# Kernel tuning notes

Hardware: AMD Instinct MI355X
Metric: run time of the kernel (lower is better)

Reference implementation:

```python
import jax, jax.numpy as jnp
import numpy as np

NN_SIZE = 10          # k for kNN (includes the point itself as its own nearest neighbor)
COS_EPS = 1e-8        # torch.nn.CosineSimilarity eps


def _pairwise_sqdist(p):
    # p: (B,N,3) -> (B,N,N) squared euclidean distances without (B,N,N,3) intermediate
    x2 = jnp.sum(p * p, axis=-1)                      # (B,N)
    inner = jnp.einsum('bnd,bmd->bnm', p, p)          # (B,N,N)
    return x2[:, :, None] + x2[:, None, :] - 2.0 * inner


def _batch_normals(points):
    # points: (B,N,3) -> PCA normals (B,N,3)
    d = _pairwise_sqdist(points)                      # (B,N,N)
    _, idx = jax.lax.top_k(-d, NN_SIZE)               # (B,N,K) indices of k nearest
    nbrs = jax.vmap(lambda p, i: p[i])(points, idx)   # (B,N,K,3) gathered neighborhoods
    centered = nbrs - jnp.mean(nbrs, axis=2, keepdims=True)
    cov = jnp.einsum('bnki,bnkj->bnij', centered, centered) / NN_SIZE  # (B,N,3,3)
    _, vecs = jnp.linalg.eigh(cov)                    # eigenvalues ascending
    return vecs[..., :, 0]                            # eigvec of smallest eigval = normal


def setup_inputs() -> dict:
    key = jax.random.key(0)
    k1, k2 = jax.random.split(key)
    pred = jax.random.normal(k1, (8, 4096, 3), dtype=jnp.float32)
    gt_normals = jax.random.normal(k2, (8, 4096, 3), dtype=jnp.float32)
    return {"pred": pred, "gt_normals": gt_normals}


def reference(pred, gt_normals):
    pred_normals = _batch_normals(pred)                         # (B,N,3)
    dot = jnp.sum(pred_normals * gt_normals, axis=-1)           # (B,N)
    na = jnp.linalg.norm(pred_normals, axis=-1)
    nb = jnp.linalg.norm(gt_normals, axis=-1)
    cos = dot / (jnp.maximum(na, COS_EPS) * jnp.maximum(nb, COS_EPS))
    return jnp.mean(1.0 - cos)
```

## Files before the change

kernel.cpp:

```cpp
#include <hip/hip_runtime.h>
#include <math.h>


#define NPTS   4096
#define KNN    10
#define NBINS  256
#define XLO    (-5.5f)
#define INVBW  (256.0f / 11.0f)
#define W      1536
#define QPB    16
#define NB     2048
#define LISTCAP 32768

__device__ __forceinline__ unsigned int umed3(unsigned int a, unsigned int b, unsigned int c) {
    unsigned int r;
    asm("v_med3_u32 %0, %1, %2, %3" : "=v"(r) : "v"(a), "v"(b), "v"(c));
    return r;
}

__device__ __forceinline__ void sift(unsigned int nd[KNN], unsigned int key) {
#pragma unroll
    for (int t = KNN - 1; t >= 1; --t)
        nd[t] = umed3(key, nd[t - 1], nd[t]);
    nd[0] = nd[0] < key ? nd[0] : key;
}

__device__ __forceinline__ int xbin(float x) {
    int bin = (int)floorf((x - XLO) * INVBW);
    return bin < 0 ? 0 : (bin > NBINS - 1 ? NBINS - 1 : bin);
}

#define MAKE_KEY(q, c, J)                                                     \
    ({                                                                        \
        float sw_ = (q).w + (c).w;                                            \
        float dp_ = fmaf((q).x, (c).x, fmaf((q).y, (c).y, (q).z * (c).z));    \
        float d_  = fmaf(-2.0f, dp_, sw_);                                    \
        d_ = fmaxf(d_, 0.0f);                                                 \
        (__float_as_uint(d_) & 0xFFFFF000u) | (unsigned)(J);                  \
    })

__device__ float normal_loss3f(const float nbx[KNN], const float nby[KNN],
                               const float nbz[KNN], const float* g3)
{
    float sx = 0.f, sy = 0.f, sz = 0.f;
#pragma unroll
    for (int t = 0; t < KNN; ++t) { sx += nbx[t]; sy += nby[t]; sz += nbz[t]; }
    float mx = sx * 0.1f, my = sy * 0.1f, mz = sz * 0.1f;
    float c00 = 0.f, c01 = 0.f, c02 = 0.f, c11 = 0.f, c12 = 0.f, c22 = 0.f;
#pragma unroll
    for (int t = 0; t < KNN; ++t) {
        float ux = nbx[t] - mx, uy = nby[t] - my, uz = nbz[t] - mz;
        c00 = fmaf(ux, ux, c00);
        c01 = fmaf(ux, uy, c01);
        c02 = fmaf(ux, uz, c02);
        c11 = fmaf(uy, uy, c11);
        c12 = fmaf(uy, uz, c12);
        c22 = fmaf(uz, uz, c22);
    }
    float a00 = c00 * 0.1f, a01 = c01 * 0.1f, a02 = c02 * 0.1f;
    float a11 = c11 * 0.1f, a12 = c12 * 0.1f, a22 = c22 * 0.1f;

    float vx = 1.0f, vy = 0.0f, vz = 0.0f;
    float qd = (a00 + a11 + a22) * (1.0f / 3.0f);
    float p1 = a01 * a01 + a02 * a02 + a12 * a12;
    float b00 = a00 - qd, b11 = a11 - qd, b22 = a22 - qd;
    float p2 = b00 * b00 + b11 * b11 + b22 * b22 + 2.0f * p1;
    if (p2 > 1e-30f) {
        float p   = sqrtf(p2 * (1.0f / 6.0f));
        float inv = 1.0f / p;
        float m00 = b00 * inv, m01 = a01 * inv, m02 = a02 * inv;
        float m11 = b11 * inv, m12 = a12 * inv, m22 = b22 * inv;
        float detB = m00 * (m11 * m22 - m12 * m12)
                   - m01 * (m01 * m22 - m12 * m02)
                   + m02 * (m01 * m12 - m11 * m02);
        float r = 0.5f * detB;
        r = r < -1.0f ? -1.0f : (r > 1.0f ? 1.0f : r);
        float phi  = acosf(r) * (1.0f / 3.0f);
        float eig0 = qd + 2.0f * p * cosf(phi + 2.0943951023931953f);
        float r0x = a00 - eig0, r0y = a01, r0z = a02;
        float r1y = a11 - eig0, r1z = a12;
        float r2z = a22 - eig0;
        float c0x = r0y * r1z - r0z * r1y;
        float c0y = r0z * r0y - r0x * r1z;
        float c0z = r0x * r1y - r0y * r0y;
        float c1x = r0y * r2z - r0z * r1z;
        float c1y = r0z * r0z - r0x * r2z;
        float c1z = r0x * r1z - r0y * r0z;
        float c2x = r1y * r2z - r1z * r1z;
        float c2y = r1z * r0z - r0y * r2z;
        float c2z = r0y * r1z - r1y * r0z;
        float n0 = c0x * c0x + c0y * c0y + c0z * c0z;
        float n1 = c1x * c1x + c1y * c1y + c1z * c1z;
        float n2 = c2x * c2x + c2y * c2y + c2z * c2z;
        float bx, by, bz, bn;
        if (n0 >= n1 && n0 >= n2) { bx = c0x; by = c0y; bz = c0z; bn = n0; }
        else if (n1 >= n2)        { bx = c1x; by = c1y; bz = c1z; bn = n1; }
        else                      { bx = c2x; by = c2y; bz = c2z; bn = n2; }
        if (bn > 1e-30f) {
            float s = rsqrtf(bn);
            vx = bx * s; vy = by * s; vz = bz * s;
        }
    }
    float gx = g3[0], gy = g3[1], gz = g3[2];
    float dotg = vx * gx + vy * gy + vz * gz;
    float na = sqrtf(vx * vx + vy * vy + vz * vz);
    float gn = sqrtf(gx * gx + gy * gy + gz * gz);
    float cs = dotg / (fmaxf(na, 1e-8f) * fmaxf(gn, 1e-8f));
    return 1.0f - cs;
}

__global__ __launch_bounds__(1024) void gtnl_bin(
    const float* __restrict__ pred, float4* __restrict__ wsPts,
    unsigned int* __restrict__ wsBins, unsigned int* __restrict__ wsCnt)
{
    __shared__ unsigned int hist[NBINS];
    __shared__ unsigned int bst[NBINS + 1];

    const int tid = threadIdx.x;
    const int b   = blockIdx.x;
    if (b == 0 && tid == 0) wsCnt[0] = 0;
    const float* src = pred + (size_t)b * NPTS * 3;

    if (tid < NBINS) hist[tid] = 0;
    __syncthreads();

    float px[4], py[4], pz[4];
    int   pb[4], pidx[4];
#pragma unroll
    for (int k = 0; k < 4; ++k) {
        int p = tid + 1024 * k;
        float x = src[3 * p + 0];
        float y = src[3 * p + 1];
        float z = src[3 * p + 2];
        int bin = xbin(x);
        px[k] = x; py[k] = y; pz[k] = z; pb[k] = bin; pidx[k] = p;
        atomicAdd(&hist[bin], 1u);
    }
    __syncthreads();

    if (tid < 64) {
        unsigned s0 = hist[4 * tid + 0], s1 = hist[4 * tid + 1];
        unsigned s2 = hist[4 * tid + 2], s3 = hist[4 * tid + 3];
        unsigned tot = s0 + s1 + s2 + s3;
        unsigned pre = tot;
#pragma unroll
        for (int d = 1; d < 64; d <<= 1) {
            unsigned t = __shfl_up(pre, d, 64);
            if (tid >= d) pre += t;
        }
        unsigned ex = pre - tot;
        bst[4 * tid + 0] = ex;
        bst[4 * tid + 1] = ex + s0;
        bst[4 * tid + 2] = ex + s0 + s1;
        bst[4 * tid + 3] = ex + s0 + s1 + s2;
        if (tid == 63) bst[NBINS] = ex + tot;
    }
    __syncthreads();

    if (tid < NBINS) hist[tid] = bst[tid];
    __syncthreads();

#pragma unroll
    for (int k = 0; k < 4; ++k) {
        unsigned pos = atomicAdd(&hist[pb[k]], 1u);
        wsPts[(size_t)b * NPTS + pos] =
            make_float4(px[k], py[k], pz[k], __uint_as_float((unsigned)pidx[k]));
    }
    if (tid < NBINS) wsBins[b * (NBINS + 1) + tid] = bst[tid];
    if (tid == 0)    wsBins[b * (NBINS + 1) + NBINS] = bst[NBINS];
}

__global__ __launch_bounds__(256, 6) void gtnl_scan(
    const float4* __restrict__ wsPts, const float* __restrict__ gt,
    float* __restrict__ qloss, unsigned int* __restrict__ wsCnt,
    unsigned int* __restrict__ wsList, float* __restrict__ wsThr)
{
    __shared__ float4 pts[W];

    const int tid   = threadIdx.x;
    const int bid   = blockIdx.x;
    const int b     = bid >> 8;
    const int chunk = bid & 255;
    const int qbase = chunk * QPB;
    const int s     = tid & 15;
    const int ql    = tid >> 4;

    int W0 = qbase + QPB / 2 - W / 2;
    W0 = W0 < 0 ? 0 : (W0 > NPTS - W ? NPTS - W : W0);

    const float4* wp = wsPts + (size_t)b * NPTS;
    for (int i = tid; i < W; i += 256) {
        float4 v = wp[W0 + i];
        pts[i] = make_float4(v.x, v.y, v.z, fmaf(v.x, v.x, fmaf(v.y, v.y, v.z * v.z)));
    }
    __syncthreads();

    const int qpos = qbase + ql;
    const float4 q = pts[qpos - W0];

    unsigned int nd[KNN];
#pragma unroll
    for (int t = 0; t < KNN; ++t) nd[t] = 0x7F000000u;

#pragma unroll 8
    for (int t = 0; t < W / 16; ++t) {
        int j = 16 * t + s;
        float4 c = pts[j];
        sift(nd, MAKE_KEY(q, c, j));
    }

#pragma unroll
    for (int r = 1; r <= 8; r <<= 1) {
        unsigned int tmp[KNN];
#pragma unroll
        for (int t = 0; t < KNN; ++t) tmp[t] = nd[t];
#pragma unroll
        for (int t = 0; t < KNN; ++t) {
            unsigned int pk = (unsigned int)__shfl_xor((int)tmp[t], r, 64);
            sift(nd, pk);
        }
    }

    unsigned int thr_bits = (nd[KNN - 1] & 0xFFFFF000u) + 0x1000u;
    float thr = __uint_as_float(thr_bits);
    float hw  = __uint_as_float(__float_as_uint(sqrtf(thr)) + 4) + 1e-3f;
    bool okL = (W0 == 0)        || (q.x - hw > pts[0].x);
    bool okR = (W0 == NPTS - W) || (q.x + hw < pts[W - 1].x);

    const unsigned int qorig = __float_as_uint(wp[qpos].w);
    if (okL && okR) {
        float nbx[KNN], nby[KNN], nbz[KNN];
#pragma unroll
        for (int t = 0; t < KNN; ++t) {
            float4 pn = pts[nd[t] & 0xFFFu];
            nbx[t] = pn.x; nby[t] = pn.y; nbz[t] = pn.z;
        }
        float res = normal_loss3f(nbx, nby, nbz, gt + ((size_t)b * NPTS + qorig) * 3);
        if (s == 0) qloss[(size_t)b * NPTS + qorig] = res;
    } else {
        if (s == 0) {
            unsigned int idx = atomicAdd(wsCnt, 1u);
            wsList[idx] = ((unsigned)b << 12) | (unsigned)qpos;
            wsThr[idx]  = hw;
            qloss[(size_t)b * NPTS + qorig] = 0.0f;
        }
    }
}

__global__ __launch_bounds__(256, 4) void gtnl_fix(
    const float4* __restrict__ wsPts, const unsigned int* __restrict__ wsBins,
    const float* __restrict__ gt, float* __restrict__ qloss,
    const unsigned int* __restrict__ wsCnt, const unsigned int* __restrict__ wsList,
    const float* __restrict__ wsThr)
{
    const int lane = threadIdx.x & 63;
    const int wid  = blockIdx.x * 4 + (threadIdx.x >> 6);
    unsigned int n = wsCnt[0];

    for (unsigned int i = wid; i < n; i += 4096) {
        unsigned int e = wsList[i];
        const int b    = e >> 12;
        const int qpos = e & 0xFFF;
        const float hw = wsThr[i];
        const float4* wp = wsPts + (size_t)b * NPTS;
        const unsigned int* bst = wsBins + b * (NBINS + 1);

        float4 qv = wp[qpos];
        float4 q  = make_float4(qv.x, qv.y, qv.z,
                                fmaf(qv.x, qv.x, fmaf(qv.y, qv.y, qv.z * qv.z)));
        const unsigned int qorig = __float_as_uint(qv.w);

        const int jlo = (int)bst[xbin(qv.x - hw)];
        const int jhi = (int)bst[xbin(qv.x + hw) + 1];

        unsigned int nd[KNN];
#pragma unroll
        for (int t = 0; t < KNN; ++t) nd[t] = 0x7F000000u;

        for (int j0 = jlo; j0 < jhi; j0 += 64) {
            int j = j0 + lane;
            int js = j < jhi ? j : jhi - 1;
            float4 v = wp[js];
            float4 c = make_float4(v.x, v.y, v.z,
                                   fmaf(v.x, v.x, fmaf(v.y, v.y, v.z * v.z)));
            unsigned int key = MAKE_KEY(q, c, js);
            key = j < jhi ? key : 0xFFFFFFFFu;
            sift(nd, key);
        }

        unsigned int keys[KNN];
#pragma unroll
        for (int r = 0; r < KNN; ++r) {
            unsigned int m = nd[0];
#pragma unroll
            for (int d = 1; d < 64; d <<= 1) {
                unsigned int o = __shfl_xor(m, d, 64);
                m = m < o ? m : o;
            }
            keys[r] = m;
            bool win = (nd[0] == m);
#pragma unroll
            for (int t = 0; t < KNN - 1; ++t) nd[t] = win ? nd[t + 1] : nd[t];
            nd[KNN - 1] = win ? 0xFFFFFFFFu : nd[KNN - 1];
        }

        float nbx[KNN], nby[KNN], nbz[KNN];
#pragma unroll
        for (int t = 0; t < KNN; ++t) {
            float4 pn = wp[keys[t] & 0xFFFu];
            nbx[t] = pn.x; nby[t] = pn.y; nbz[t] = pn.z;
        }
        float res = normal_loss3f(nbx, nby, nbz, gt + ((size_t)b * NPTS + qorig) * 3);
        if (lane == 0) qloss[(size_t)b * NPTS + qorig] = res;
    }
}

__global__ __launch_bounds__(1024) void gtnl_reduceQ(
    const float* __restrict__ qloss, float* __restrict__ out)
{
    __shared__ float sbuf[1024];
    const int tid = threadIdx.x;
    const float4* q4 = (const float4*)qloss;
    float s = 0.0f;
#pragma unroll
    for (int t = 0; t < 8; ++t) {
        float4 v = q4[tid + 1024 * t];
        s += (v.x + v.y) + (v.z + v.w);
    }
    sbuf[tid] = s;
    __syncthreads();
    for (int k = 512; k > 0; k >>= 1) {
        if (tid < k) sbuf[tid] += sbuf[tid + k];
        __syncthreads();
    }
    if (tid == 0) out[0] = sbuf[0] / 32768.0f;
}

__global__ __launch_bounds__(256) void gtnl_brute(
    const float* __restrict__ pred, const float* __restrict__ gt,
    float* __restrict__ partial)
{
    __shared__ float4 ptsB[NPTS];
    __shared__ unsigned int mbuf[64][3][KNN];

    const int tid = threadIdx.x;
    const int b   = blockIdx.x >> 6;
    const int qc  = blockIdx.x & 63;
    const int ql  = tid & 63;
    const int sub = tid >> 6;
    const int qi  = qc * 64 + ql;

    const float* src = pred + (size_t)b * NPTS * 3;
    for (int p = tid; p < NPTS; p += 256) {
        float x = src[3 * p + 0], y = src[3 * p + 1], z = src[3 * p + 2];
        ptsB[p] = make_float4(x, y, z, fmaf(x, x, fmaf(y, y, z * z)));
    }
    __syncthreads();

    const float4 q = ptsB[qi];
    unsigned int nd[KNN];
#pragma unroll
    for (int t = 0; t < KNN; ++t) nd[t] = 0xFFFFFFFFu;

    const int j0 = sub * 1024;
#pragma unroll 8
    for (int j = j0; j < j0 + 1024; ++j) {
        float4 c = ptsB[j];
        sift(nd, MAKE_KEY(q, c, j));
    }

    if (sub != 0) {
#pragma unroll
        for (int t = 0; t < KNN; ++t) mbuf[ql][sub - 1][t] = nd[t];
    }
    __syncthreads();

    float res = 0.0f;
    if (sub == 0) {
#pragma unroll
        for (int ss = 0; ss < 3; ++ss)
#pragma unroll
            for (int t = 0; t < KNN; ++t) sift(nd, mbuf[ql][ss][t]);
        float nbx[KNN], nby[KNN], nbz[KNN];
#pragma unroll
        for (int t = 0; t < KNN; ++t) {
            float4 pn = ptsB[nd[t] & 0xFFFu];
            nbx[t] = pn.x; nby[t] = pn.y; nbz[t] = pn.z;
        }
        res = normal_loss3f(nbx, nby, nbz, gt + ((size_t)b * NPTS + qi) * 3);
#pragma unroll
        for (int d = 32; d > 0; d >>= 1) res += __shfl_xor(res, d, 64);
    }
    __syncthreads();
    if (tid == 0) partial[blockIdx.x] = res;
}

__global__ __launch_bounds__(512) void gtnl_reduceP(
    const float* __restrict__ partial, float* __restrict__ out)
{
    __shared__ float sb[512];
    const int tid = threadIdx.x;
    sb[tid] = partial[tid];
    __syncthreads();
    for (int k = 256; k > 0; k >>= 1) {
        if (tid < k) sb[tid] += sb[tid + k];
        __syncthreads();
    }
    if (tid == 0) out[0] = sb[0] / 32768.0f;
}

extern "C" void kernel_launch(void* const* d_in, const int* in_sizes, int n_in,
                              void* d_out, int out_size, void* d_ws, size_t ws_size,
                              hipStream_t stream) {
    const float* pred = (const float*)d_in[0];
    const float* gt   = (const float*)d_in[1];
    float* out        = (float*)d_out;

    const size_t PTS_BYTES   = (size_t)8 * NPTS * sizeof(float4);
    const size_t QLOSS_BYTES = (size_t)8 * NPTS * sizeof(float);
    const size_t LIST_BYTES  = (size_t)LISTCAP * sizeof(unsigned);
    const size_t THR_BYTES   = (size_t)LISTCAP * sizeof(float);
    const size_t BINS_BYTES  = (size_t)8 * (NBINS + 1) * sizeof(unsigned);
    const size_t NEED = PTS_BYTES + QLOSS_BYTES + LIST_BYTES + THR_BYTES + BINS_BYTES + 64;

    if (ws_size >= NEED) {
        char* p = (char*)d_ws;
        float4*       wsPts  = (float4*)p;                 p += PTS_BYTES;
        float*        qloss  = (float*)p;                  p += QLOSS_BYTES;
        unsigned int* wsList = (unsigned int*)p;           p += LIST_BYTES;
        float*        wsThr  = (float*)p;                  p += THR_BYTES;
        unsigned int* wsBins = (unsigned int*)p;           p += BINS_BYTES;
        unsigned int* wsCnt  = (unsigned int*)p;

        gtnl_bin<<<8, 1024, 0, stream>>>(pred, wsPts, wsBins, wsCnt);
        gtnl_scan<<<NB, 256, 0, stream>>>(wsPts, gt, qloss, wsCnt, wsList, wsThr);
        gtnl_fix<<<1024, 256, 0, stream>>>(wsPts, wsBins, gt, qloss, wsCnt, wsList, wsThr);
        gtnl_reduceQ<<<1, 1024, 0, stream>>>(qloss, out);
    } else {
        float* partial = (float*)d_ws;
        gtnl_brute<<<512, 256, 0, stream>>>(pred, gt, partial);
        gtnl_reduceP<<<1, 512, 0, stream>>>(partial, out);
    }
}
```

Before: 61.28 us.

## Use 6-deep per-lane top-k with 8 lanes per query and direct distances

The scan kernel now gives each query 8 lanes instead of 16 and keeps only the 6 best candidates per lane, which shortens the sorting network. A validity check sends a query to the fix path whenever a lane's sixth-best key could still have hidden neighbours. Distances are now computed directly as squared differences, replacing the norm-expansion form, and per-query loss is stored at the sorted position, not the original index. The aim is to cut ALU work per candidate, at the risk of more queries going to the slower fix kernel.

Result: faster. 54.71 us (-10.7%).

```diff
diff --git a/kernel.cpp b/kernel.cpp
--- a/kernel.cpp
+++ b/kernel.cpp
@@ -4,12 +4,13 @@
 
 #define NPTS   4096
 #define KNN    10
+#define KEEP   6
 #define NBINS  256
 #define XLO    (-5.5f)
 #define INVBW  (256.0f / 11.0f)
 #define W      1536
-#define QPB    16
-#define NB     2048
+#define QPB    32
+#define NB     1024
 #define LISTCAP 32768
 
 __device__ __forceinline__ unsigned int umed3(unsigned int a, unsigned int b, unsigned int c) {
@@ -25,19 +26,17 @@
     nd[0] = nd[0] < key ? nd[0] : key;
 }
 
+__device__ __forceinline__ void sift6(unsigned int nd[KEEP], unsigned int key) {
+#pragma unroll
+    for (int t = KEEP - 1; t >= 1; --t)
+        nd[t] = umed3(key, nd[t - 1], nd[t]);
+    nd[0] = nd[0] < key ? nd[0] : key;
+}
+
 __device__ __forceinline__ int xbin(float x) {
     int bin = (int)floorf((x - XLO) * INVBW);
     return bin < 0 ? 0 : (bin > NBINS - 1 ? NBINS - 1 : bin);
 }
-
-#define MAKE_KEY(q, c, J)                                                     \
-    ({                                                                        \
-        float sw_ = (q).w + (c).w;                                            \
-        float dp_ = fmaf((q).x, (c).x, fmaf((q).y, (c).y, (q).z * (c).z));    \
-        float d_  = fmaf(-2.0f, dp_, sw_);                                    \
-        d_ = fmaxf(d_, 0.0f);                                                 \
-        (__float_as_uint(d_) & 0xFFFFF000u) | (unsigned)(J);                  \
-    })
 
 __device__ float normal_loss3f(const float nbx[KNN], const float nby[KNN],
                                const float nbz[KNN], const float* g3)
@@ -179,38 +178,44 @@
 
     const int tid   = threadIdx.x;
     const int bid   = blockIdx.x;
-    const int b     = bid >> 8;
-    const int chunk = bid & 255;
+    const int b     = bid >> 7;
+    const int chunk = bid & 127;
     const int qbase = chunk * QPB;
-    const int s     = tid & 15;
-    const int ql    = tid >> 4;
+    const int s     = tid & 7;
+    const int ql    = tid >> 3;
 
     int W0 = qbase + QPB / 2 - W / 2;
     W0 = W0 < 0 ? 0 : (W0 > NPTS - W ? NPTS - W : W0);
 
     const float4* wp = wsPts + (size_t)b * NPTS;
-    for (int i = tid; i < W; i += 256) {
-        float4 v = wp[W0 + i];
-        pts[i] = make_float4(v.x, v.y, v.z, fmaf(v.x, v.x, fmaf(v.y, v.y, v.z * v.z)));
-    }
+    for (int i = tid; i < W; i += 256) pts[i] = wp[W0 + i];
     __syncthreads();
 
     const int qpos = qbase + ql;
     const float4 q = pts[qpos - W0];
 
+    unsigned int nd6[KEEP];
+#pragma unroll
+    for (int t = 0; t < KEEP; ++t) nd6[t] = 0x7F000000u;
+
+    int j = s;
+#pragma unroll 8
+    for (int t = 0; t < W / 8; ++t, j += 8) {
+        float4 c = pts[j];
+        float dx = q.x - c.x, dy = q.y - c.y, dz = q.z - c.z;
+        float d  = fmaf(dx, dx, fmaf(dy, dy, dz * dz));
+        unsigned int key = (__float_as_uint(d) & 0xFFFFF000u) | (unsigned)j;
+        sift6(nd6, key);
+    }
+    const unsigned int kmin6 = nd6[KEEP - 1];
+
     unsigned int nd[KNN];
 #pragma unroll
-    for (int t = 0; t < KNN; ++t) nd[t] = 0x7F000000u;
-
-#pragma unroll 8
-    for (int t = 0; t < W / 16; ++t) {
-        int j = 16 * t + s;
-        float4 c = pts[j];
-        sift(nd, MAKE_KEY(q, c, j));
-    }
-
-#pragma unroll
-    for (int r = 1; r <= 8; r <<= 1) {
+    for (int t = 0; t < KEEP; ++t) nd[t] = nd6[t];
+#pragma unroll
+    for (int t = KEEP; t < KNN; ++t) nd[t] = 0x7F000000u;
+#pragma unroll
+    for (int r = 1; r <= 4; r <<= 1) {
         unsigned int tmp[KNN];
 #pragma unroll
         for (int t = 0; t < KNN; ++t) tmp[t] = nd[t];
@@ -220,6 +225,10 @@
             sift(nd, pk);
         }
     }
+
+    unsigned int sok = (kmin6 > nd[KNN - 1]) ? 1u : 0u;
+#pragma unroll
+    for (int r = 1; r <= 4; r <<= 1) sok &= (unsigned int)__shfl_xor((int)sok, r, 64);
 
     unsigned int thr_bits = (nd[KNN - 1] & 0xFFFFF000u) + 0x1000u;
     float thr = __uint_as_float(thr_bits);
@@ -227,23 +236,21 @@
     bool okL = (W0 == 0)        || (q.x - hw > pts[0].x);
     bool okR = (W0 == NPTS - W) || (q.x + hw < pts[W - 1].x);
 
-    const unsigned int qorig = __float_as_uint(wp[qpos].w);
-    if (okL && okR) {
+    if (okL && okR && sok) {
         float nbx[KNN], nby[KNN], nbz[KNN];
 #pragma unroll
         for (int t = 0; t < KNN; ++t) {
             float4 pn = pts[nd[t] & 0xFFFu];
             nbx[t] = pn.x; nby[t] = pn.y; nbz[t] = pn.z;
         }
+        const unsigned int qorig = __float_as_uint(q.w);
         float res = normal_loss3f(nbx, nby, nbz, gt + ((size_t)b * NPTS + qorig) * 3);
-        if (s == 0) qloss[(size_t)b * NPTS + qorig] = res;
-    } else {
-        if (s == 0) {
-            unsigned int idx = atomicAdd(wsCnt, 1u);
-            wsList[idx] = ((unsigned)b << 12) | (unsigned)qpos;
-            wsThr[idx]  = hw;
-            qloss[(size_t)b * NPTS + qorig] = 0.0f;
-        }
+        if (s == 0) qloss[(size_t)b * NPTS + qpos] = res;
+    } else if (s == 0) {
+        unsigned int idx = atomicAdd(wsCnt, 1u);
+        wsList[idx] = ((unsigned)b << 12) | (unsigned)qpos;
+        wsThr[idx]  = hw;
+        qloss[(size_t)b * NPTS + qpos] = 0.0f;
     }
 }
 
@@ -266,8 +273,6 @@
         const unsigned int* bst = wsBins + b * (NBINS + 1);
 
         float4 qv = wp[qpos];
-        float4 q  = make_float4(qv.x, qv.y, qv.z,
-                                fmaf(qv.x, qv.x, fmaf(qv.y, qv.y, qv.z * qv.z)));
         const unsigned int qorig = __float_as_uint(qv.w);
 
         const int jlo = (int)bst[xbin(qv.x - hw)];
@@ -281,9 +286,9 @@
             int j = j0 + lane;
             int js = j < jhi ? j : jhi - 1;
             float4 v = wp[js];
-            float4 c = make_float4(v.x, v.y, v.z,
-                                   fmaf(v.x, v.x, fmaf(v.y, v.y, v.z * v.z)));
-            unsigned int key = MAKE_KEY(q, c, js);
+            float dx = qv.x - v.x, dy = qv.y - v.y, dz = qv.z - v.z;
+            float d  = fmaf(dx, dx, fmaf(dy, dy, dz * dz));
+            unsigned int key = (__float_as_uint(d) & 0xFFFFF000u) | (unsigned)js;
             key = j < jhi ? key : 0xFFFFFFFFu;
             sift(nd, key);
         }
@@ -311,7 +316,7 @@
             nbx[t] = pn.x; nby[t] = pn.y; nbz[t] = pn.z;
         }
         float res = normal_loss3f(nbx, nby, nbz, gt + ((size_t)b * NPTS + qorig) * 3);
-        if (lane == 0) qloss[(size_t)b * NPTS + qorig] = res;
+        if (lane == 0) qloss[(size_t)b * NPTS + qpos] = res;
     }
 }
 
@@ -353,7 +358,7 @@
     const float* src = pred + (size_t)b * NPTS * 3;
     for (int p = tid; p < NPTS; p += 256) {
         float x = src[3 * p + 0], y = src[3 * p + 1], z = src[3 * p + 2];
-        ptsB[p] = make_float4(x, y, z, fmaf(x, x, fmaf(y, y, z * z)));
+        ptsB[p] = make_float4(x, y, z, 0.0f);
     }
     __syncthreads();
 
@@ -366,7 +371,9 @@
 #pragma unroll 8
     for (int j = j0; j < j0 + 1024; ++j) {
         float4 c = ptsB[j];
-        sift(nd, MAKE_KEY(q, c, j));
+        float dx = q.x - c.x, dy = q.y - c.y, dz = q.z - c.z;
+        float d  = fmaf(dx, dx, fmaf(dy, dy, dz * dz));
+        sift(nd, (__float_as_uint(d) & 0xFFFFF000u) | (unsigned)j);
     }
 
     if (sub != 0) {
```
